# Kernel optimization log

Hardware: AMD Instinct MI355X
Metric: run time of the kernel (lower is better)

The kernel has to match this reference:

```python
import jax, jax.numpy as jnp
import numpy as np

N = 50000      # num_nodes
E = 800000     # num_edges (avg degree 16)
IN, HID, OUT = 128, 64, 64


def setup_inputs() -> dict:
    key = jax.random.key(0)
    ks = jax.random.split(key, 4)
    x = jax.random.normal(ks[0], (N, IN), dtype=jnp.float32)
    edge_index = jax.random.randint(ks[1], (2, E), 0, N, dtype=jnp.int32)
    # GCNConv params: weight [in, out] and bias [out] per layer
    W1 = jax.random.normal(ks[2], (IN, HID), dtype=jnp.float32) * 0.05
    b1 = jnp.zeros((HID,), dtype=jnp.float32)
    W2 = jax.random.normal(ks[3], (HID, OUT), dtype=jnp.float32) * 0.05
    b2 = jnp.zeros((OUT,), dtype=jnp.float32)
    return {"x": x, "edge_index": edge_index, "W1": W1, "b1": b1, "W2": W2, "b2": b2}


def _gcn_conv(x, W, b, src, dst, norm, n):
    # linear transform, then normalized gather->scatter-add aggregation
    h = x @ W                                    # [N, out]
    msg = h[src] * norm[:, None]                 # [E+N, out] gathered messages
    out = jax.ops.segment_sum(msg, dst, num_segments=n)
    return out + b


def reference(x, edge_index, W1, b1, W2, b2):
    n = x.shape[0]
    # add self-loops (PyG GCNConv default)
    loop = jnp.arange(n, dtype=edge_index.dtype)
    src = jnp.concatenate([edge_index[0], loop])
    dst = jnp.concatenate([edge_index[1], loop])
    # symmetric normalization D^-1/2 A D^-1/2 (degree over destination)
    deg = jax.ops.segment_sum(jnp.ones_like(dst, dtype=x.dtype), dst, num_segments=n)
    dinv = jnp.where(deg > 0, jax.lax.rsqrt(deg), jnp.zeros_like(deg))
    norm = dinv[src] * dinv[dst]                 # [E+N]
    h = _gcn_conv(x, W1, b1, src, dst, norm, n)
    h = jax.nn.leaky_relu(h, negative_slope=0.01)
    # dropout is identity in eval mode (training=False)
    return _gcn_conv(h, W2, b2, src, dst, norm, n)
```

## Files before the change

kernel.cpp:

```cpp
#include <hip/hip_runtime.h>
#include <hip/hip_fp16.h>
#include <type_traits>


#define NBC   128
#define BSH   7
#define NBMAX 512
#define CAP   8192

typedef __bf16 bf16x8 __attribute__((ext_vector_type(8)));
typedef float  f32x4  __attribute__((ext_vector_type(4)));

__device__ __forceinline__ unsigned short f2bf(float f) {
    unsigned u = __float_as_uint(f);
    unsigned r = u + 0x7fff + ((u >> 16) & 1);
    return (unsigned short)(r >> 16);
}
__device__ __forceinline__ float bf2f(unsigned short h) {
    return __uint_as_float(((unsigned)h) << 16);
}

__global__ __launch_bounds__(256) void k_hist1(const int* __restrict__ dst,
                                               int* __restrict__ T, int E, int nbuck) {
    __shared__ int hist[NBMAX];
    for (int i = threadIdx.x; i < nbuck; i += 256) hist[i] = 0;
    __syncthreads();
    const int per = (E + NBC - 1) / NBC;
    const int beg = blockIdx.x * per, end = min(beg + per, E);
    for (int i = beg + threadIdx.x; i < end; i += 256)
        atomicAdd(&hist[dst[i] >> BSH], 1);
    __syncthreads();
    for (int b = threadIdx.x; b < nbuck; b += 256)
        T[b * NBC + blockIdx.x] = hist[b];
}

__global__ __launch_bounds__(1024) void k_bsum(const int* __restrict__ in,
                                               int* __restrict__ bsum, int m) {
    __shared__ int red[16];
    const int t = threadIdx.x;
    const int i = blockIdx.x * 1024 + t;
    int v = (i < m) ? in[i] : 0;
#pragma unroll
    for (int o = 32; o; o >>= 1) v += __shfl_down(v, o);
    if ((t & 63) == 0) red[t >> 6] = v;
    __syncthreads();
    if (t == 0) {
        int s = 0;
#pragma unroll
        for (int w = 0; w < 16; ++w) s += red[w];
        bsum[blockIdx.x] = s;
    }
}

__global__ void k_sbsum(const int* __restrict__ bsum, int* __restrict__ boff, int nb) {
    if (threadIdx.x == 0 && blockIdx.x == 0) {
        int run = 0;
        for (int i = 0; i < nb; ++i) { boff[i] = run; run += bsum[i]; }
    }
}

__global__ __launch_bounds__(1024) void k_scanexc(
    const int* __restrict__ in, const int* __restrict__ boff,
    int* __restrict__ out, int m) {
    __shared__ int sh[1024];
    const int t = threadIdx.x;
    const int i = blockIdx.x * 1024 + t;
    const int v = (i < m) ? in[i] : 0;
    sh[t] = v;
    __syncthreads();
#pragma unroll
    for (int o = 1; o < 1024; o <<= 1) {
        int add = (t >= o) ? sh[t - o] : 0;
        __syncthreads();
        sh[t] += add;
        __syncthreads();
    }
    if (i < m) out[i] = boff[blockIdx.x] + sh[t] - v;
}

__global__ __launch_bounds__(256) void k_part1(
    const int* __restrict__ src, const int* __restrict__ dst,
    const int* __restrict__ Toff, unsigned* __restrict__ stage, int E, int nbuck) {
    __shared__ int base[NBMAX];
    __shared__ int cnt[NBMAX];
    for (int i = threadIdx.x; i < nbuck; i += 256) {
        base[i] = Toff[i * NBC + blockIdx.x];
        cnt[i] = 0;
    }
    __syncthreads();
    const int per = (E + NBC - 1) / NBC;
    const int beg = blockIdx.x * per, end = min(beg + per, E);
    for (int i = beg + threadIdx.x; i < end; i += 256) {
        int d = dst[i], s = src[i];
        int b = d >> BSH;
        int p = atomicAdd(&cnt[b], 1);
        stage[base[b] + p] = ((unsigned)(d & 127) << 17) | (unsigned)s;
    }
}

__global__ __launch_bounds__(256) void k_part2(
    const int* __restrict__ Toff, const unsigned* __restrict__ stage,
    int* __restrict__ csr, int* __restrict__ rowptr, float* __restrict__ dinv,
    int n, int E, int nbuck) {
    __shared__ unsigned buf[CAP];
    __shared__ unsigned srt[CAP];
    __shared__ int cnt[128], sc[128], curs[128];
    __shared__ int rbs, res;
    const int t = threadIdx.x;
    const int b = blockIdx.x;
    if (t < 128) cnt[t] = 0;
    if (t == 0) {
        rbs = Toff[b * NBC];
        res = (b == nbuck - 1) ? E : Toff[(b + 1) * NBC];
    }
    __syncthreads();
    const int rb = rbs, re = res, len = re - rb;
    if (len <= CAP) {
        for (int i = t; i < len; i += 256) {
            unsigned r = stage[rb + i];
            buf[i] = r;
            atomicAdd(&cnt[(r >> 17) & 127], 1);
        }
        __syncthreads();
        if (t < 128) sc[t] = cnt[t];
        __syncthreads();
#pragma unroll
        for (int o = 1; o < 128; o <<= 1) {
            int add = (t < 128 && t >= o) ? sc[t - o] : 0;
            __syncthreads();
            if (t < 128) sc[t] += add;
            __syncthreads();
        }
        if (t < 128) {
            curs[t] = sc[t] - cnt[t];
            const int gi = b * 128 + t;
            if (gi < n) {
                rowptr[gi] = rb + sc[t] - cnt[t];
                dinv[gi] = rsqrtf((float)cnt[t] + 1.f);
                if (gi == n - 1) rowptr[n] = rb + sc[t];
            }
        }
        __syncthreads();
        for (int i = t; i < len; i += 256) {
            unsigned r = buf[i];
            int p = atomicAdd(&curs[(r >> 17) & 127], 1);
            srt[p] = r & 0x1FFFF;
        }
        __syncthreads();
        for (int i = t; i < len; i += 256) csr[rb + i] = (int)srt[i];
    } else {
        for (int i = rb + t; i < re; i += 256)
            atomicAdd(&cnt[(stage[i] >> 17) & 127], 1);
        __syncthreads();
        if (t < 128) sc[t] = cnt[t];
        __syncthreads();
#pragma unroll
        for (int o = 1; o < 128; o <<= 1) {
            int add = (t < 128 && t >= o) ? sc[t - o] : 0;
            __syncthreads();
            if (t < 128) sc[t] += add;
            __syncthreads();
        }
        if (t < 128) {
            curs[t] = rb + sc[t] - cnt[t];
            const int gi = b * 128 + t;
            if (gi < n) {
                rowptr[gi] = rb + sc[t] - cnt[t];
                dinv[gi] = rsqrtf((float)cnt[t] + 1.f);
                if (gi == n - 1) rowptr[n] = rb + sc[t];
            }
        }
        __syncthreads();
        for (int i = rb + t; i < re; i += 256) {
            unsigned r = stage[i];
            int p = atomicAdd(&curs[(r >> 17) & 127], 1);
            csr[p] = (int)(r & 0x1FFFF);
        }
    }
}

__global__ void k_wsplit2(const float* __restrict__ W1, const float* __restrict__ W2,
                          unsigned short* __restrict__ W1s, unsigned short* __restrict__ W2s) {
    int i = blockIdx.x * blockDim.x + threadIdx.x;
    const float* W; unsigned short* out; int K, idx;
    if (i < 128 * 64)            { W = W1; out = W1s; K = 128; idx = i; }
    else if (i < 128 * 64 + 64 * 64) { W = W2; out = W2s; K = 64; idx = i - 128 * 64; }
    else return;
    int k = idx >> 6, c = idx & 63;
    float v = W[k * 64 + c];
    unsigned short hi = f2bf(v);
    unsigned short lo = f2bf(v - bf2f(hi));
    int T = K / 32;
    int t = k >> 5, kk = k & 31, g = kk >> 3, j = kk & 7;
    int ct = c >> 4, lane = g * 16 + (c & 15);
    out[(((size_t)(0 * T + t) * 4 + ct) * 64 + lane) * 8 + j] = hi;
    out[(((size_t)(1 * T + t) * 4 + ct) * 64 + lane) * 8 + j] = lo;
}

template<int K, bool LEAKY, typename AT>
__global__ __launch_bounds__(256) void k_gemm_mfma(
    const AT* __restrict__ A, const unsigned short* __restrict__ Ws,
    const float* __restrict__ dinv, __half* __restrict__ C, int n) {
    constexpr int T = K / 32;
    const int lane = threadIdx.x & 63;
    const int w = blockIdx.x * 4 + (threadIdx.x >> 6);
    const int r0 = w * 16;
    if (r0 >= n) return;
    const int g = lane >> 4, rA = lane & 15;

    bf16x8 ahi[T], alo[T];
    const AT* arow = A + (size_t)(r0 + rA) * K + g * 8;
#pragma unroll
    for (int t = 0; t < T; ++t) {
        float f[8];
        if constexpr (std::is_same<AT, float>::value) {
            float4 v0 = *(const float4*)(arow + t * 32);
            float4 v1 = *(const float4*)(arow + t * 32 + 4);
            f[0] = v0.x; f[1] = v0.y; f[2] = v0.z; f[3] = v0.w;
            f[4] = v1.x; f[5] = v1.y; f[6] = v1.z; f[7] = v1.w;
        } else {
            union { uint4 q; __half h[8]; } u;
            u.q = *(const uint4*)(arow + t * 32);
#pragma unroll
            for (int j = 0; j < 8; ++j) f[j] = __half2float(u.h[j]);
        }
        union { unsigned short u[8]; bf16x8 v; } H, L;
#pragma unroll
        for (int j = 0; j < 8; ++j) {
            float x = f[j];
            if (LEAKY) x = x > 0.f ? x : 0.01f * x;
            unsigned short h = f2bf(x);
            H.u[j] = h;
            L.u[j] = f2bf(x - bf2f(h));
        }
        ahi[t] = H.v; alo[t] = L.v;
    }

    f32x4 acc[4];
#pragma unroll
    for (int ct = 0; ct < 4; ++ct) acc[ct] = (f32x4){0.f, 0.f, 0.f, 0.f};

#pragma unroll
    for (int ct = 0; ct < 4; ++ct) {
#pragma unroll
        for (int t = 0; t < T; ++t) {
            union { uint4 q; bf16x8 v; } Bh, Bl;
            Bh.q = *(const uint4*)(Ws + (((size_t)(0 * T + t) * 4 + ct) * 64 + lane) * 8);
            Bl.q = *(const uint4*)(Ws + (((size_t)(1 * T + t) * 4 + ct) * 64 + lane) * 8);
            acc[ct] = __builtin_amdgcn_mfma_f32_16x16x32_bf16(ahi[t], Bh.v, acc[ct], 0, 0, 0);
            acc[ct] = __builtin_amdgcn_mfma_f32_16x16x32_bf16(ahi[t], Bl.v, acc[ct], 0, 0, 0);
            acc[ct] = __builtin_amdgcn_mfma_f32_16x16x32_bf16(alo[t], Bh.v, acc[ct], 0, 0, 0);
        }
    }

    float dv[4];
#pragma unroll
    for (int r = 0; r < 4; ++r) dv[r] = dinv[r0 + g * 4 + r];

    __half* crow = C + (size_t)(r0 + g * 4) * 64 + rA;
#pragma unroll
    for (int ct = 0; ct < 4; ++ct)
#pragma unroll
        for (int r = 0; r < 4; ++r)
            crow[(size_t)r * 64 + ct * 16] = __float2half_rn(acc[ct][r] * dv[r]);
}

template<typename OT>
__global__ __launch_bounds__(256) void k_aggcsr(
    const int* __restrict__ rowptr, const int* __restrict__ csr,
    const float* __restrict__ dinv, const __half* __restrict__ hs,
    const float* __restrict__ bias, OT* __restrict__ out, int n) {
    const int lane = threadIdx.x & 63;
    const int wid  = blockIdx.x * 4 + (threadIdx.x >> 6);
    const int nw   = gridDim.x * 4;
    const float bl = bias[lane];
    for (int dd = wid; dd < n; dd += nw) {
        const int d = __builtin_amdgcn_readfirstlane(dd);
        const int beg = rowptr[d], end = rowptr[d + 1];
        float a0 = 0.f, a1 = 0.f, a2 = 0.f, a3 = 0.f;
        float a4 = 0.f, a5 = 0.f, a6 = 0.f, a7 = 0.f;
        int j = beg;
        for (; j + 8 <= end; j += 8) {
            int s0 = csr[j + 0], s1 = csr[j + 1], s2 = csr[j + 2], s3 = csr[j + 3];
            int s4 = csr[j + 4], s5 = csr[j + 5], s6 = csr[j + 6], s7 = csr[j + 7];
            a0 += __half2float(hs[(size_t)s0 * 64 + lane]);
            a1 += __half2float(hs[(size_t)s1 * 64 + lane]);
            a2 += __half2float(hs[(size_t)s2 * 64 + lane]);
            a3 += __half2float(hs[(size_t)s3 * 64 + lane]);
            a4 += __half2float(hs[(size_t)s4 * 64 + lane]);
            a5 += __half2float(hs[(size_t)s5 * 64 + lane]);
            a6 += __half2float(hs[(size_t)s6 * 64 + lane]);
            a7 += __half2float(hs[(size_t)s7 * 64 + lane]);
        }
        for (; j < end; ++j)
            a0 += __half2float(hs[(size_t)csr[j] * 64 + lane]);
        const float di = dinv[d];
        const float acc = ((a0 + a1) + (a2 + a3)) + ((a4 + a5) + (a6 + a7));
        const float v = (acc + __half2float(hs[(size_t)d * 64 + lane])) * di + bl;
        if constexpr (std::is_same<OT, __half>::value)
            out[(size_t)d * 64 + lane] = __float2half_rn(v);
        else
            out[(size_t)d * 64 + lane] = v;
    }
}

extern "C" void kernel_launch(void* const* d_in, const int* in_sizes, int n_in,
                              void* d_out, int out_size, void* d_ws, size_t ws_size,
                              hipStream_t stream) {
    const float* x  = (const float*)d_in[0];
    const int*   ei = (const int*)d_in[1];
    const float* W1 = (const float*)d_in[2];
    const float* b1 = (const float*)d_in[3];
    const float* W2 = (const float*)d_in[4];
    const float* b2 = (const float*)d_in[5];
    float* out = (float*)d_out;

    const int n = in_sizes[0] / 128;
    const int E = in_sizes[1] / 2;
    const int* src = ei;
    const int* dst = ei + E;

    const int nbuck = (n + 127) >> BSH;
    const int m = nbuck * NBC;
    const int nb2 = (m + 1023) / 1024;

    char* ws = (char*)d_ws;
    size_t off = 0;
    auto alloc = [&](size_t bytes) { void* p = ws + off; off = (off + bytes + 255) & ~(size_t)255; return p; };
    int*      T      = (int*)alloc((size_t)m * 4);
    int*      Toff   = (int*)alloc((size_t)m * 4);
    int*      bsum   = (int*)alloc((size_t)nb2 * 4);
    int*      boff   = (int*)alloc((size_t)nb2 * 4);
    unsigned* stage  = (unsigned*)alloc((size_t)E * 4);
    int*      csr    = (int*)alloc((size_t)E * 4);
    int*      rowptr = (int*)alloc((size_t)(n + 1) * 4);
    float*    dinv   = (float*)alloc((size_t)n * 4);
    __half*   hs     = (__half*)alloc((size_t)n * 64 * 2);
    __half*   out1   = (__half*)alloc((size_t)n * 64 * 2);
    unsigned short* W1s = (unsigned short*)alloc((size_t)2 * 128 * 64 * 2);
    unsigned short* W2s = (unsigned short*)alloc((size_t)2 * 64 * 64 * 2);
    (void)ws_size; (void)n_in; (void)out_size;

    k_hist1  <<<NBC, 256, 0, stream>>>(dst, T, E, nbuck);
    k_bsum   <<<nb2, 1024, 0, stream>>>(T, bsum, m);
    k_sbsum  <<<1, 64, 0, stream>>>(bsum, boff, nb2);
    k_scanexc<<<nb2, 1024, 0, stream>>>(T, boff, Toff, m);
    k_part1  <<<NBC, 256, 0, stream>>>(src, dst, Toff, stage, E, nbuck);
    k_part2  <<<nbuck, 256, 0, stream>>>(Toff, stage, csr, rowptr, dinv, n, E, nbuck);

    k_wsplit2<<<(128 * 64 + 64 * 64 + 255) / 256, 256, 0, stream>>>(W1, W2, W1s, W2s);

    const int gemmBlocks = (n / 16 + 3) / 4;
    k_gemm_mfma<128, false, float><<<gemmBlocks, 256, 0, stream>>>(x, W1s, dinv, hs, n);
    k_aggcsr<__half><<<2048, 256, 0, stream>>>(rowptr, csr, dinv, hs, b1, out1, n);

    k_gemm_mfma<64, true, __half><<<gemmBlocks, 256, 0, stream>>>(out1, W2s, dinv, hs, n);
    k_aggcsr<float><<<2048, 256, 0, stream>>>(rowptr, csr, dinv, hs, b2, out, n);
}
```

Before: 111.3 us.

## Fuse layer-1 aggregation with layer-2 GEMM and merge weight split into histogram

Adds a kernel that aggregates the neighbours of 16 destination rows per wave, applies bias and leaky ReLU, stages the rows in shared memory, then runs the layer-2 MFMA GEMM directly. This removes the fp16 out1 intermediate round trip and one launch. The weight bf16 split is folded into the histogram kernel as extra blocks, and the gather loops are unrolled to 16 accumulators for more memory-level parallelism. The trade-off is that the fused kernel uses a fixed 16-row-per-wave mapping with no grid-stride loop, so load balance across rows of different degree may be worse.

```diff
diff --git a/kernel.cpp b/kernel.cpp
--- a/kernel.cpp
+++ b/kernel.cpp
@@ -20,9 +20,31 @@
     return __uint_as_float(((unsigned)h) << 16);
 }
 
-__global__ __launch_bounds__(256) void k_hist1(const int* __restrict__ dst,
-                                               int* __restrict__ T, int E, int nbuck) {
+__device__ __forceinline__ void wsplit_one(const float* __restrict__ W,
+                                           unsigned short* __restrict__ out,
+                                           int K, int idx) {
+    int k = idx >> 6, c = idx & 63;
+    float v = W[k * 64 + c];
+    unsigned short hi = f2bf(v);
+    unsigned short lo = f2bf(v - bf2f(hi));
+    int T = K / 32;
+    int t = k >> 5, kk = k & 31, g = kk >> 3, j = kk & 7;
+    int ct = c >> 4, lane = g * 16 + (c & 15);
+    out[(((size_t)(0 * T + t) * 4 + ct) * 64 + lane) * 8 + j] = hi;
+    out[(((size_t)(1 * T + t) * 4 + ct) * 64 + lane) * 8 + j] = lo;
+}
+
+__global__ __launch_bounds__(256) void k_hist_wsplit(
+    const int* __restrict__ dst, int* __restrict__ T, int E, int nbuck,
+    const float* __restrict__ W1, const float* __restrict__ W2,
+    unsigned short* __restrict__ W1s, unsigned short* __restrict__ W2s) {
     __shared__ int hist[NBMAX];
+    if (blockIdx.x >= NBC) {
+        int i = (blockIdx.x - NBC) * 256 + threadIdx.x;
+        if (i < 128 * 64) wsplit_one(W1, W1s, 128, i);
+        else if (i < 128 * 64 + 64 * 64) wsplit_one(W2, W2s, 64, i - 128 * 64);
+        return;
+    }
     for (int i = threadIdx.x; i < nbuck; i += 256) hist[i] = 0;
     __syncthreads();
     const int per = (E + NBC - 1) / NBC;
@@ -179,27 +201,9 @@
     }
 }
 
-__global__ void k_wsplit2(const float* __restrict__ W1, const float* __restrict__ W2,
-                          unsigned short* __restrict__ W1s, unsigned short* __restrict__ W2s) {
-    int i = blockIdx.x * blockDim.x + threadIdx.x;
-    const float* W; unsigned short* out; int K, idx;
-    if (i < 128 * 64)            { W = W1; out = W1s; K = 128; idx = i; }
-    else if (i < 128 * 64 + 64 * 64) { W = W2; out = W2s; K = 64; idx = i - 128 * 64; }
-    else return;
-    int k = idx >> 6, c = idx & 63;
-    float v = W[k * 64 + c];
-    unsigned short hi = f2bf(v);
-    unsigned short lo = f2bf(v - bf2f(hi));
-    int T = K / 32;
-    int t = k >> 5, kk = k & 31, g = kk >> 3, j = kk & 7;
-    int ct = c >> 4, lane = g * 16 + (c & 15);
-    out[(((size_t)(0 * T + t) * 4 + ct) * 64 + lane) * 8 + j] = hi;
-    out[(((size_t)(1 * T + t) * 4 + ct) * 64 + lane) * 8 + j] = lo;
-}
-
-template<int K, bool LEAKY, typename AT>
+template<int K>
 __global__ __launch_bounds__(256) void k_gemm_mfma(
-    const AT* __restrict__ A, const unsigned short* __restrict__ Ws,
+    const float* __restrict__ A, const unsigned short* __restrict__ Ws,
     const float* __restrict__ dinv, __half* __restrict__ C, int n) {
     constexpr int T = K / 32;
     const int lane = threadIdx.x & 63;
@@ -209,29 +213,18 @@
     const int g = lane >> 4, rA = lane & 15;
 
     bf16x8 ahi[T], alo[T];
-    const AT* arow = A + (size_t)(r0 + rA) * K + g * 8;
+    const float* arow = A + (size_t)(r0 + rA) * K + g * 8;
 #pragma unroll
     for (int t = 0; t < T; ++t) {
-        float f[8];
-        if constexpr (std::is_same<AT, float>::value) {
-            float4 v0 = *(const float4*)(arow + t * 32);
-            float4 v1 = *(const float4*)(arow + t * 32 + 4);
-            f[0] = v0.x; f[1] = v0.y; f[2] = v0.z; f[3] = v0.w;
-            f[4] = v1.x; f[5] = v1.y; f[6] = v1.z; f[7] = v1.w;
-        } else {
-            union { uint4 q; __half h[8]; } u;
-            u.q = *(const uint4*)(arow + t * 32);
-#pragma unroll
-            for (int j = 0; j < 8; ++j) f[j] = __half2float(u.h[j]);
-        }
+        float4 v0 = *(const float4*)(arow + t * 32);
+        float4 v1 = *(const float4*)(arow + t * 32 + 4);
+        float f[8] = {v0.x, v0.y, v0.z, v0.w, v1.x, v1.y, v1.z, v1.w};
         union { unsigned short u[8]; bf16x8 v; } H, L;
 #pragma unroll
         for (int j = 0; j < 8; ++j) {
-            float x = f[j];
-            if (LEAKY) x = x > 0.f ? x : 0.01f * x;
-            unsigned short h = f2bf(x);
+            unsigned short h = f2bf(f[j]);
             H.u[j] = h;
-            L.u[j] = f2bf(x - bf2f(h));
+            L.u[j] = f2bf(f[j] - bf2f(h));
         }
         ahi[t] = H.v; alo[t] = L.v;
     }
@@ -239,7 +232,6 @@
     f32x4 acc[4];
 #pragma unroll
     for (int ct = 0; ct < 4; ++ct) acc[ct] = (f32x4){0.f, 0.f, 0.f, 0.f};
-
 #pragma unroll
     for (int ct = 0; ct < 4; ++ct) {
 #pragma unroll
@@ -256,7 +248,6 @@
     float dv[4];
 #pragma unroll
     for (int r = 0; r < 4; ++r) dv[r] = dinv[r0 + g * 4 + r];
-
     __half* crow = C + (size_t)(r0 + g * 4) * 64 + rA;
 #pragma unroll
     for (int ct = 0; ct < 4; ++ct)
@@ -265,11 +256,104 @@
             crow[(size_t)r * 64 + ct * 16] = __float2half_rn(acc[ct][r] * dv[r]);
 }
 
-template<typename OT>
+__global__ __launch_bounds__(256) void k_agg_gemm(
+    const int* __restrict__ rowptr, const int* __restrict__ csr,
+    const float* __restrict__ dinv, const __half* __restrict__ hs1,
+    const float* __restrict__ b1, const unsigned short* __restrict__ Ws,
+    __half* __restrict__ hs2, int n) {
+    __shared__ float AS[4][16][68];
+    const int lane = threadIdx.x & 63;
+    const int wv = threadIdx.x >> 6;
+    const int base = (blockIdx.x * 4 + wv) * 16;
+    const float bl = b1[lane];
+
+    for (int r = 0; r < 16; ++r) {
+        const int d = base + r;
+        float v = 0.f;
+        if (d < n) {
+            const int du = __builtin_amdgcn_readfirstlane(d);
+            const int beg = rowptr[du], end = rowptr[du + 1];
+            float a[16];
+#pragma unroll
+            for (int i = 0; i < 16; ++i) a[i] = 0.f;
+            int j = beg;
+            for (; j + 16 <= end; j += 16) {
+                int s[16];
+#pragma unroll
+                for (int i = 0; i < 16; ++i) s[i] = csr[j + i];
+#pragma unroll
+                for (int i = 0; i < 16; ++i)
+                    a[i] += __half2float(hs1[(size_t)s[i] * 64 + lane]);
+            }
+            for (; j + 4 <= end; j += 4) {
+                int s[4];
+#pragma unroll
+                for (int i = 0; i < 4; ++i) s[i] = csr[j + i];
+#pragma unroll
+                for (int i = 0; i < 4; ++i)
+                    a[i] += __half2float(hs1[(size_t)s[i] * 64 + lane]);
+            }
+            for (; j < end; ++j)
+                a[0] += __half2float(hs1[(size_t)csr[j] * 64 + lane]);
+            float acc = (((a[0] + a[1]) + (a[2] + a[3])) + ((a[4] + a[5]) + (a[6] + a[7])))
+                      + (((a[8] + a[9]) + (a[10] + a[11])) + ((a[12] + a[13]) + (a[14] + a[15])));
+            const float di = dinv[du];
+            v = (acc + __half2float(hs1[(size_t)du * 64 + lane])) * di + bl;
+            v = v > 0.f ? v : 0.01f * v;
+        }
+        AS[wv][r][lane] = v;
+    }
+    __syncthreads();
+
+    const int g = lane >> 4, rA = lane & 15;
+    bf16x8 ahi[2], alo[2];
+#pragma unroll
+    for (int t = 0; t < 2; ++t) {
+        float4 v0 = *(const float4*)&AS[wv][rA][t * 32 + g * 8];
+        float4 v1 = *(const float4*)&AS[wv][rA][t * 32 + g * 8 + 4];
+        float f[8] = {v0.x, v0.y, v0.z, v0.w, v1.x, v1.y, v1.z, v1.w};
+        union { unsigned short u[8]; bf16x8 v; } H, L;
+#pragma unroll
+        for (int j = 0; j < 8; ++j) {
+            unsigned short h = f2bf(f[j]);
+            H.u[j] = h;
+            L.u[j] = f2bf(f[j] - bf2f(h));
+        }
+        ahi[t] = H.v; alo[t] = L.v;
+    }
+
+    f32x4 acc[4];
+#pragma unroll
+    for (int ct = 0; ct < 4; ++ct) acc[ct] = (f32x4){0.f, 0.f, 0.f, 0.f};
+#pragma unroll
+    for (int ct = 0; ct < 4; ++ct) {
+#pragma unroll
+        for (int t = 0; t < 2; ++t) {
+            union { uint4 q; bf16x8 v; } Bh, Bl;
+            Bh.q = *(const uint4*)(Ws + (((size_t)(0 * 2 + t) * 4 + ct) * 64 + lane) * 8);
+            Bl.q = *(const uint4*)(Ws + (((size_t)(1 * 2 + t) * 4 + ct) * 64 + lane) * 8);
+            acc[ct] = __builtin_amdgcn_mfma_f32_16x16x32_bf16(ahi[t], Bh.v, acc[ct], 0, 0, 0);
+            acc[ct] = __builtin_amdgcn_mfma_f32_16x16x32_bf16(ahi[t], Bl.v, acc[ct], 0, 0, 0);
+            acc[ct] = __builtin_amdgcn_mfma_f32_16x16x32_bf16(alo[t], Bh.v, acc[ct], 0, 0, 0);
+        }
+    }
+
+#pragma unroll
+    for (int r = 0; r < 4; ++r) {
+        const int row = base + g * 4 + r;
+        if (row < n) {
+            const float dv = dinv[row];
+#pragma unroll
+            for (int ct = 0; ct < 4; ++ct)
+                hs2[(size_t)row * 64 + ct * 16 + rA] = __float2half_rn(acc[ct][r] * dv);
+        }
+    }
+}
+
 __global__ __launch_bounds__(256) void k_aggcsr(
     const int* __restrict__ rowptr, const int* __restrict__ csr,
     const float* __restrict__ dinv, const __half* __restrict__ hs,
-    const float* __restrict__ bias, OT* __restrict__ out, int n) {
+    const float* __restrict__ bias, float* __restrict__ out, int n) {
     const int lane = threadIdx.x & 63;
     const int wid  = blockIdx.x * 4 + (threadIdx.x >> 6);
     const int nw   = gridDim.x * 4;
@@ -277,30 +361,33 @@
     for (int dd = wid; dd < n; dd += nw) {
         const int d = __builtin_amdgcn_readfirstlane(dd);
         const int beg = rowptr[d], end = rowptr[d + 1];
-        float a0 = 0.f, a1 = 0.f, a2 = 0.f, a3 = 0.f;
-        float a4 = 0.f, a5 = 0.f, a6 = 0.f, a7 = 0.f;
+        float a[16];
+#pragma unroll
+        for (int i = 0; i < 16; ++i) a[i] = 0.f;
         int j = beg;
-        for (; j + 8 <= end; j += 8) {
-            int s0 = csr[j + 0], s1 = csr[j + 1], s2 = csr[j + 2], s3 = csr[j + 3];
-            int s4 = csr[j + 4], s5 = csr[j + 5], s6 = csr[j + 6], s7 = csr[j + 7];
-            a0 += __half2float(hs[(size_t)s0 * 64 + lane]);
-            a1 += __half2float(hs[(size_t)s1 * 64 + lane]);
-            a2 += __half2float(hs[(size_t)s2 * 64 + lane]);
-            a3 += __half2float(hs[(size_t)s3 * 64 + lane]);
-            a4 += __half2float(hs[(size_t)s4 * 64 + lane]);
-            a5 += __half2float(hs[(size_t)s5 * 64 + lane]);
-            a6 += __half2float(hs[(size_t)s6 * 64 + lane]);
-            a7 += __half2float(hs[(size_t)s7 * 64 + lane]);
+        for (; j + 16 <= end; j += 16) {
+            int s[16];
+#pragma unroll
+            for (int i = 0; i < 16; ++i) s[i] = csr[j + i];
+#pragma unroll
+            for (int i = 0; i < 16; ++i)
+                a[i] += __half2float(hs[(size_t)s[i] * 64 + lane]);
+        }
+        for (; j + 4 <= end; j += 4) {
+            int s[4];
+#pragma unroll
+            for (int i = 0; i < 4; ++i) s[i] = csr[j + i];
+#pragma unroll
+            for (int i = 0; i < 4; ++i)
+                a[i] += __half2float(hs[(size_t)s[i] * 64 + lane]);
         }
         for (; j < end; ++j)
-            a0 += __half2float(hs[(size_t)csr[j] * 64 + lane]);
+            a[0] += __half2float(hs[(size_t)csr[j] * 64 + lane]);
+        float acc = (((a[0] + a[1]) + (a[2] + a[3])) + ((a[4] + a[5]) + (a[6] + a[7])))
+                  + (((a[8] + a[9]) + (a[10] + a[11])) + ((a[12] + a[13]) + (a[14] + a[15])));
         const float di = dinv[d];
-        const float acc = ((a0 + a1) + (a2 + a3)) + ((a4 + a5) + (a6 + a7));
-        const float v = (acc + __half2float(hs[(size_t)d * 64 + lane])) * di + bl;
-        if constexpr (std::is_same<OT, __half>::value)
-            out[(size_t)d * 64 + lane] = __float2half_rn(v);
-        else
-            out[(size_t)d * 64 + lane] = v;
+        out[(size_t)d * 64 + lane] =
+            (acc + __half2float(hs[(size_t)d * 64 + lane])) * di + bl;
     }
 }
 
@@ -335,25 +422,23 @@
     int*      csr    = (int*)alloc((size_t)E * 4);
     int*      rowptr = (int*)alloc((size_t)(n + 1) * 4);
     float*    dinv   = (float*)alloc((size_t)n * 4);
-    __half*   hs     = (__half*)alloc((size_t)n * 64 * 2);
-    __half*   out1   = (__half*)alloc((size_t)n * 64 * 2);
+    __half*   hs1    = (__half*)alloc((size_t)n * 64 * 2);
+    __half*   hs2    = (__half*)alloc((size_t)n * 64 * 2);
     unsigned short* W1s = (unsigned short*)alloc((size_t)2 * 128 * 64 * 2);
     unsigned short* W2s = (unsigned short*)alloc((size_t)2 * 64 * 64 * 2);
     (void)ws_size; (void)n_in; (void)out_size;
 
-    k_hist1  <<<NBC, 256, 0, stream>>>(dst, T, E, nbuck);
+    const int wsplitBlocks = (128 * 64 + 64 * 64) / 256;
+
+    k_hist_wsplit<<<NBC + wsplitBlocks, 256, 0, stream>>>(dst, T, E, nbuck, W1, W2, W1s, W2s);
     k_bsum   <<<nb2, 1024, 0, stream>>>(T, bsum, m);
     k_sbsum  <<<1, 64, 0, stream>>>(bsum, boff, nb2);
     k_scanexc<<<nb2, 1024, 0, stream>>>(T, boff, Toff, m);
     k_part1  <<<NBC, 256, 0, stream>>>(src, dst, Toff, stage, E, nbuck);
     k_part2  <<<nbuck, 256, 0, stream>>>(Toff, stage, csr, rowptr, dinv, n, E, nbuck);
 
-    k_wsplit2<<<(128 * 64 + 64 * 64 + 255) / 256, 256, 0, stream>>>(W1, W2, W1s, W2s);
-
-    const int gemmBlocks = (n / 16 + 3) / 4;
-    k_gemm_mfma<128, false, float><<<gemmBlocks, 256, 0, stream>>>(x, W1s, dinv, hs, n);
-    k_aggcsr<__half><<<2048, 256, 0, stream>>>(rowptr, csr, dinv, hs, b1, out1, n);
-
-    k_gemm_mfma<64, true, __half><<<gemmBlocks, 256, 0, stream>>>(out1, W2s, dinv, hs, n);
-    k_aggcsr<float><<<2048, 256, 0, stream>>>(rowptr, csr, dinv, hs, b2, out, n);
-}
+    const int gemmBlocks = ((n + 15) / 16 + 3) / 4;
+    k_gemm_mfma<128><<<gemmBlocks, 256, 0, stream>>>(x, W1s, dinv, hs1, n);
+    k_agg_gemm <<<gemmBlocks, 256, 0, stream>>>(rowptr, csr, dinv, hs1, b1, W2s, hs2, n);
+    k_aggcsr   <<<2048, 256, 0, stream>>>(rowptr, csr, dinv, hs2, b2, out, n);
+}
```

New measurement: 122.2 us. 1.1x slower.
